# Optimization experiments

Measured on AMD Instinct MI355X. Metric: run time of the kernel, lower is better.

The kernel has to match this reference:

```python
import jax, jax.numpy as jnp
import numpy as np

DIM = 768
HID = 1536
EPS = 1e-12
SCALE = float(np.sqrt(DIM))


def _layernorm(x, gamma, beta):
    mu = jnp.mean(x, axis=-1, keepdims=True)
    var = jnp.mean(jnp.square(x - mu), axis=-1, keepdims=True)
    return (x - mu) * jax.lax.rsqrt(var + EPS) * gamma + beta


def setup_inputs() -> dict:
    key = jax.random.key(0)
    ks = jax.random.split(key, 16)
    s = 1.0 / np.sqrt(DIM)
    sh = 1.0 / np.sqrt(HID)
    x = jax.random.normal(ks[0], (8, 2048, DIM), dtype=jnp.float32)
    return {
        "x": x,
        "Wq": jax.random.uniform(ks[1], (DIM, DIM), jnp.float32, -s, s),
        "bq": jax.random.uniform(ks[2], (DIM,), jnp.float32, -s, s),
        "Wk": jax.random.uniform(ks[3], (DIM, DIM), jnp.float32, -s, s),
        "bk": jax.random.uniform(ks[4], (DIM,), jnp.float32, -s, s),
        "Wv": jax.random.uniform(ks[5], (DIM, DIM), jnp.float32, -s, s),
        "bv": jax.random.uniform(ks[6], (DIM,), jnp.float32, -s, s),
        "Wp": jax.random.uniform(ks[7], (DIM, DIM), jnp.float32, -s, s),
        "bp": jax.random.uniform(ks[8], (DIM,), jnp.float32, -s, s),
        "g1": jnp.ones((DIM,), jnp.float32),
        "be1": jnp.zeros((DIM,), jnp.float32),
        "W1": jax.random.uniform(ks[9], (HID, DIM), jnp.float32, -s, s),
        "b1": jax.random.uniform(ks[10], (HID,), jnp.float32, -s, s),
        "W2": jax.random.uniform(ks[11], (DIM, HID), jnp.float32, -sh, sh),
        "b2": jax.random.uniform(ks[12], (DIM,), jnp.float32, -sh, sh),
        "g2": jnp.ones((DIM,), jnp.float32),
        "be2": jnp.zeros((DIM,), jnp.float32),
    }


def reference(x, Wq, bq, Wk, bk, Wv, bv, Wp, bp, g1, be1, W1, b1, W2, b2, g2, be2):
    # NOTE: original code does NOT split into heads; single full-dim bmm attention.
    Q = jnp.einsum("bsd,ed->bse", x, Wq) + bq  # [B,S,D]
    K = jnp.einsum("bsd,ed->bse", x, Wk) + bk
    V = jnp.einsum("bsd,ed->bse", x, Wv) + bv
    alpha = jnp.einsum("bqd,bkd->bqk", Q, K) / SCALE  # [B,S,S]
    alpha = jax.nn.softmax(alpha, axis=-1)
    attn = jnp.einsum("bqk,bkd->bqd", alpha, V)
    attn = jnp.einsum("bsd,ed->bse", attn, Wp) + bp  # linear_proj
    h = _layernorm(x + attn, g1, be1)
    mlp = jax.nn.gelu(jnp.einsum("bsd,hd->bsh", h, W1) + b1, approximate=False)
    mlp = jnp.einsum("bsh,dh->bsd", mlp, W2) + b2
    return _layernorm(h + mlp, g2, be2)
```

## Files before the change

kernel.cpp:

```cpp
#include <hip/hip_runtime.h>
#include <math.h>

#define D_MODEL 768
#define D_HID   1536
#define N_BATCH 8
#define SEQLEN  2048
#define NROWS   (N_BATCH*SEQLEN)

typedef unsigned short u16;
typedef __attribute__((ext_vector_type(8))) short bfrag;
typedef __attribute__((ext_vector_type(4))) float facc;

__device__ __forceinline__ u16 f2bf(float f) {
  unsigned u = __float_as_uint(f);
  u += 0x7fffu + ((u >> 16) & 1u);
  return (u16)(u >> 16);
}

__device__ __forceinline__ void async16(const void* g, void* l) {
  __builtin_amdgcn_global_load_lds((const __attribute__((address_space(1))) void*)g,
                                   (__attribute__((address_space(3))) void*)l,
                                   16, 0, 0);
}

__global__ __launch_bounds__(256) void cvt_all(
    const float* __restrict__ x,  const float* __restrict__ Wq,
    const float* __restrict__ Wk, const float* __restrict__ Wv,
    const float* __restrict__ Wp, const float* __restrict__ W1,
    const float* __restrict__ W2, const float* __restrict__ bq,
    const float* __restrict__ bk, const float* __restrict__ bv,
    u16* __restrict__ XB, u16* __restrict__ WQKV, u16* __restrict__ WPB,
    u16* __restrict__ W1B, u16* __restrict__ W2B, float* __restrict__ BQKV) {
  long i = (long)blockIdx.x * 256 + threadIdx.x;
  const float* src; u16* dst; long off;
  if      (i < 3145728) { src = x;  dst = XB;             off = i; }
  else if (i < 3293184) { src = Wq; dst = WQKV;           off = i - 3145728; }
  else if (i < 3440640) { src = Wk; dst = WQKV + 589824;  off = i - 3293184; }
  else if (i < 3588096) { src = Wv; dst = WQKV + 1179648; off = i - 3440640; }
  else if (i < 3735552) { src = Wp; dst = WPB;            off = i - 3588096; }
  else if (i < 4030464) { src = W1; dst = W1B;            off = i - 3735552; }
  else if (i < 4325376) { src = W2; dst = W2B;            off = i - 4030464; }
  else if (i < 4325952) {
    long j = i - 4325376;
    const float* s = (j < 192) ? bq : (j < 384) ? bk : bv;
    long o = (j < 192) ? j : (j < 384) ? j - 192 : j - 384;
    ((float4*)BQKV)[j] = ((const float4*)s)[o];
    return;
  } else return;
  float4 v = ((const float4*)src)[off];
  ushort4 o4;
  o4.x = f2bf(v.x); o4.y = f2bf(v.y); o4.z = f2bf(v.z); o4.w = f2bf(v.w);
  *reinterpret_cast<ushort4*>(dst + off * 4) = o4;
}

__global__ __launch_bounds__(256) void transpose_bf16(const u16* __restrict__ in,
                                                      u16* __restrict__ out) {
  __shared__ u16 t[64][68];
  const int z  = blockIdx.z;
  const int bs = blockIdx.x * 64;
  const int bd = blockIdx.y * 64;
  const u16* I = in  + (long)z * SEQLEN * D_MODEL;
  u16*       O = out + (long)z * D_MODEL * SEQLEN;
  const int tt = threadIdx.x;
  const int r = tt >> 2, c4 = (tt & 3) << 4;
#pragma unroll
  for (int k = 0; k < 16; ++k)
    t[r][c4 + k] = I[(long)(bs + r) * D_MODEL + bd + c4 + k];
  __syncthreads();
#pragma unroll
  for (int k = 0; k < 16; ++k)
    O[(long)(bd + r) * SEQLEN + bs + c4 + k] = t[c4 + k][r];
}

enum { EPI_BIAS = 0, EPI_EXP = 1, EPI_DIV = 2, EPI_BIASX = 3, EPI_GELU = 4, EPI_QKV = 5 };

template<int EPI>
__global__ __launch_bounds__(512, 4)
void gemm_bt(const u16* __restrict__ Aall, const u16* __restrict__ Ball,
             void* __restrict__ Cout,
             int M, int N, int K,
             long sA, long sB, long sC,
             const float* __restrict__ bias,
             const float* __restrict__ xadd,
             float* __restrict__ lsum,
             float scale)
{
  __shared__ __align__(16) char smem[65536];
  u16* As = (u16*)smem;
  u16* Bs = (u16*)(smem + 16384);

  const int z = blockIdx.z;
  const u16* A = Aall + (long)z * sA;
  const u16* B = Ball + (long)z * sB;
  const int bm = blockIdx.x, bn = blockIdx.y;
  const int tid = (int)threadIdx.x;
  const int lane = tid & 63, wv = tid >> 6;
  const int wr = wv >> 2, wc = wv & 3;

  facc acc[4][4] = {};

  const int srow = tid >> 3;
  const int scol = (((tid & 7) ^ (srow & 7)) << 3);
  const u16* Abase = A + (long)(bm * 128) * K;
  const u16* Bbase = B + (long)(bn * 256) * K;

  const int fr = lane & 15;
  const int g0 = lane >> 4;

  for (int k0 = 0; k0 < K; k0 += 64) {
    __syncthreads();
#pragma unroll
    for (int p = 0; p < 2; ++p)
      async16(Abase + (long)(p * 64 + srow) * K + k0 + scol, As + (p * 512 + wv * 64) * 8);
#pragma unroll
    for (int p = 0; p < 4; ++p)
      async16(Bbase + (long)(p * 64 + srow) * K + k0 + scol, Bs + (p * 512 + wv * 64) * 8);
    __syncthreads();
#pragma unroll
    for (int h = 0; h < 2; ++h) {
      bfrag af[4], bfv[4];
      const int gh = g0 + h * 4;
      const int cs = (gh ^ (fr & 7)) << 3;
#pragma unroll
      for (int i = 0; i < 4; ++i) {
        const int r = wr * 64 + i * 16 + fr;
        af[i] = *(const bfrag*)(As + r * 64 + ((gh ^ (r & 7)) << 3));
      }
#pragma unroll
      for (int j = 0; j < 4; ++j) {
        const int r = wc * 64 + j * 16 + fr;
        bfv[j] = *(const bfrag*)(Bs + r * 64 + ((gh ^ (r & 7)) << 3));
      }
      (void)cs;
#pragma unroll
      for (int i = 0; i < 4; ++i)
#pragma unroll
        for (int j = 0; j < 4; ++j)
          acc[i][j] = __builtin_amdgcn_mfma_f32_16x16x32_bf16(af[i], bfv[j], acc[i][j], 0, 0, 0);
    }
  }

  __syncthreads();
  const int rb = bm * 128 + wr * 64;
  const int cb = bn * 256 + wc * 64;
  const int quad = lane >> 4;

  if constexpr (EPI == EPI_BIASX) {
    float* ep32 = (float*)(smem + wv * 8192);
    float* Cg = (float*)Cout + (long)z * sC;
#pragma unroll
    for (int h = 0; h < 2; ++h) {
#pragma unroll
      for (int i2 = 0; i2 < 2; ++i2) {
        const int i = h * 2 + i2;
#pragma unroll
        for (int r = 0; r < 4; ++r) {
          const int lrow = i2 * 16 + quad * 4 + r;
#pragma unroll
          for (int j = 0; j < 4; ++j)
            ep32[lrow * 64 + j * 16 + fr] = acc[i][j][r];
        }
      }
#pragma unroll
      for (int it = 0; it < 8; ++it) {
        const int lr = it * 4 + (lane >> 4);
        const int ch = (lane & 15) << 2;
        float4 d = *(const float4*)(ep32 + lr * 64 + ch);
        const int gcol = cb + ch;
        const long gi = (long)(rb + h * 32 + lr) * N + gcol;
        const float4 xa = *(const float4*)(xadd + gi);
        const float4 bb = *(const float4*)(bias + gcol);
        d.x += xa.x + bb.x; d.y += xa.y + bb.y; d.z += xa.z + bb.z; d.w += xa.w + bb.w;
        *(float4*)(Cg + gi) = d;
      }
    }
  } else {
    u16* ep16 = (u16*)(smem + wv * 8192);
    u16* Cg;
    int cbo;
    int rowstride;
    if constexpr (EPI == EPI_QKV) {
      const int c64 = bn * 4 + wc;
      const int which = c64 / 12;
      Cg = (u16*)Cout + (long)which * NROWS * D_MODEL;
      cbo = (c64 - which * 12) * 64;
      rowstride = D_MODEL;
    } else {
      Cg = (u16*)Cout + (long)z * sC;
      cbo = cb;
      rowstride = N;
    }
    float bj[4];
    if constexpr (EPI == EPI_BIAS || EPI == EPI_GELU || EPI == EPI_QKV) {
#pragma unroll
      for (int j = 0; j < 4; ++j) bj[j] = bias[cb + j * 16 + fr];
    }
#pragma unroll
    for (int i = 0; i < 4; ++i) {
#pragma unroll
      for (int r = 0; r < 4; ++r) {
        const int lrow = i * 16 + quad * 4 + r;
        const int row = rb + lrow;
        float rs = 0.f;
        float inv = 0.f;
        if constexpr (EPI == EPI_DIV) inv = 1.f / lsum[(long)z * M + row];
#pragma unroll
        for (int j = 0; j < 4; ++j) {
          float v = acc[i][j][r];
          float outv;
          if constexpr (EPI == EPI_EXP) {
            outv = __expf(v * scale);
            rs += outv;
          } else if constexpr (EPI == EPI_DIV) {
            outv = v * inv;
          } else if constexpr (EPI == EPI_BIAS || EPI == EPI_QKV) {
            outv = v + bj[j];
          } else {
            float t = v + bj[j];
            outv = 0.5f * t * (1.f + erff(t * 0.70710678f));
          }
          ep16[lrow * 64 + j * 16 + fr] = f2bf(outv);
        }
        if constexpr (EPI == EPI_EXP) {
          rs += __shfl_xor(rs, 1);
          rs += __shfl_xor(rs, 2);
          rs += __shfl_xor(rs, 4);
          rs += __shfl_xor(rs, 8);
          if (fr == 0) atomicAdd(&lsum[(long)z * M + row], rs);
        }
      }
    }
#pragma unroll
    for (int it = 0; it < 8; ++it) {
      const int lr = it * 8 + (lane >> 3);
      const int ch = (lane & 7) << 3;
      int4 d = *(const int4*)(ep16 + lr * 64 + ch);
      *reinterpret_cast<int4*>(Cg + (long)(rb + lr) * rowstride + cbo + ch) = d;
    }
  }
}

__global__ __launch_bounds__(256) void layernorm_rows(const float* __restrict__ in,
                                                      const float* __restrict__ gamma,
                                                      const float* __restrict__ beta,
                                                      float* __restrict__ outf,
                                                      u16* __restrict__ outb) {
  const int row = blockIdx.x;
  const float* p = in + (long)row * D_MODEL;
  const int t = threadIdx.x;
  float v0 = p[t], v1 = p[t + 256], v2 = p[t + 512];
  float s1 = v0 + v1 + v2;
  float s2 = v0 * v0 + v1 * v1 + v2 * v2;
#pragma unroll
  for (int o = 32; o; o >>= 1) { s1 += __shfl_xor(s1, o); s2 += __shfl_xor(s2, o); }
  __shared__ float r1[4], r2[4];
  const int wv = t >> 6, ln = t & 63;
  if (ln == 0) { r1[wv] = s1; r2[wv] = s2; }
  __syncthreads();
  s1 = r1[0] + r1[1] + r1[2] + r1[3];
  s2 = r2[0] + r2[1] + r2[2] + r2[3];
  const float mu = s1 * (1.f / 768.f);
  const float var = s2 * (1.f / 768.f) - mu * mu;
  const float rstd = rsqrtf(var + 1e-12f);
  float g0 = gamma[t], g1v = gamma[t + 256], g2v = gamma[t + 512];
  float b0 = beta[t],  b1v = beta[t + 256],  b2v = beta[t + 512];
  float o0 = (v0 - mu) * rstd * g0 + b0;
  float o1 = (v1 - mu) * rstd * g1v + b1v;
  float o2 = (v2 - mu) * rstd * g2v + b2v;
  float* q = outf + (long)row * D_MODEL;
  q[t] = o0; q[t + 256] = o1; q[t + 512] = o2;
  if (outb) {
    u16* qb = outb + (long)row * D_MODEL;
    qb[t] = f2bf(o0); qb[t + 256] = f2bf(o1); qb[t + 512] = f2bf(o2);
  }
}

static const size_t OFF_WP   = 0;
static const size_t OFF_W1   = 1179648;
static const size_t OFF_W2   = 3538944;
static const size_t OFF_LSUM = 5898240;
static const size_t OFF_BQKV = 5963776;
static const size_t OFF_QB   = 6291456;
static const size_t OFF_KB   = 31457280;
static const size_t OFF_VB   = 56623104;
static const size_t OFF_VT   = 81788928;
static const size_t OFF_EB   = 106954752;
static const size_t OFF_XB   = 174063616;
static const size_t OFF_WQKV = 199229440;

extern "C" void kernel_launch(void* const* d_in, const int* in_sizes, int n_in,
                              void* d_out, int out_size, void* d_ws, size_t ws_size,
                              hipStream_t stream) {
  const float* x   = (const float*)d_in[0];
  const float* Wq  = (const float*)d_in[1];
  const float* bq  = (const float*)d_in[2];
  const float* Wk  = (const float*)d_in[3];
  const float* bk  = (const float*)d_in[4];
  const float* Wv  = (const float*)d_in[5];
  const float* bv  = (const float*)d_in[6];
  const float* Wp  = (const float*)d_in[7];
  const float* bp  = (const float*)d_in[8];
  const float* g1  = (const float*)d_in[9];
  const float* be1 = (const float*)d_in[10];
  const float* W1  = (const float*)d_in[11];
  const float* b1  = (const float*)d_in[12];
  const float* W2  = (const float*)d_in[13];
  const float* b2  = (const float*)d_in[14];
  const float* g2  = (const float*)d_in[15];
  const float* be2 = (const float*)d_in[16];

  char* ws = (char*)d_ws;
  u16*   WPB  = (u16*)(ws + OFF_WP);
  u16*   W1B  = (u16*)(ws + OFF_W1);
  u16*   W2B  = (u16*)(ws + OFF_W2);
  float* LSUM = (float*)(ws + OFF_LSUM);
  float* BQKV = (float*)(ws + OFF_BQKV);
  u16*   QB   = (u16*)(ws + OFF_QB);
  u16*   KB   = (u16*)(ws + OFF_KB);
  u16*   VB   = (u16*)(ws + OFF_VB);
  u16*   VT   = (u16*)(ws + OFF_VT);
  u16*   EB   = (u16*)(ws + OFF_EB);
  u16*   XB   = (u16*)(ws + OFF_XB);
  u16*   WQKV = (u16*)(ws + OFF_WQKV);
  u16*   CTX  = (u16*)(ws + OFF_XB);
  float* PF   = (float*)(ws + OFF_QB);
  float* HF   = (float*)(ws + OFF_VB);
  u16*   HB   = (u16*)(ws + OFF_EB);
  u16*   M1B  = (u16*)(ws + OFF_QB);
  float* M2F  = (float*)(ws + OFF_EB);

  dim3 blk(256), blkg(512);

  cvt_all<<<dim3(16899), blk, 0, stream>>>(x, Wq, Wk, Wv, Wp, W1, W2, bq, bk, bv,
                                           XB, WQKV, WPB, W1B, W2B, BQKV);
  hipMemsetAsync(LSUM, 0, NROWS * sizeof(float), stream);

  gemm_bt<EPI_QKV><<<dim3(128, 9, 1), blkg, 0, stream>>>(XB, WQKV, QB,
      NROWS, 3 * D_MODEL, D_MODEL, 0, 0, 0, BQKV, nullptr, nullptr, 0.f);
  transpose_bf16<<<dim3(SEQLEN / 64, D_MODEL / 64, N_BATCH), blk, 0, stream>>>(VB, VT);

  const float sc = 1.0f / sqrtf((float)D_MODEL);
  gemm_bt<EPI_EXP><<<dim3(16, 8, 8), blkg, 0, stream>>>(QB, KB, EB,
      SEQLEN, SEQLEN, D_MODEL,
      (long)SEQLEN * D_MODEL, (long)SEQLEN * D_MODEL, (long)SEQLEN * SEQLEN,
      nullptr, nullptr, LSUM, sc);
  gemm_bt<EPI_DIV><<<dim3(16, 3, 8), blkg, 0, stream>>>(EB, VT, CTX,
      SEQLEN, D_MODEL, SEQLEN,
      (long)SEQLEN * SEQLEN, (long)D_MODEL * SEQLEN, (long)SEQLEN * D_MODEL,
      nullptr, nullptr, LSUM, 0.f);
  gemm_bt<EPI_BIASX><<<dim3(128, 3, 1), blkg, 0, stream>>>(CTX, WPB, PF,
      NROWS, D_MODEL, D_MODEL, 0, 0, 0, bp, x, nullptr, 0.f);
  layernorm_rows<<<dim3(NROWS), blk, 0, stream>>>(PF, g1, be1, HF, HB);
  gemm_bt<EPI_GELU><<<dim3(128, 6, 1), blkg, 0, stream>>>(HB, W1B, M1B,
      NROWS, D_HID, D_MODEL, 0, 0, 0, b1, nullptr, nullptr, 0.f);
  gemm_bt<EPI_BIASX><<<dim3(128, 3, 1), blkg, 0, stream>>>(M1B, W2B, M2F,
      NROWS, D_MODEL, D_HID, 0, 0, 0, b2, HF, nullptr, 0.f);
  layernorm_rows<<<dim3(NROWS), blk, 0, stream>>>(M2F, g2, be2, (float*)d_out, nullptr);

  (void)in_sizes; (void)n_in; (void)out_size; (void)ws_size;
}
```

Before: 518.4 us.

## Use 32x32x16 MFMA, bf16 residual intermediates, and vectorized layernorm

Switches the GEMM inner loop from 16x16x32 to 32x32x16 bf16 MFMA with 2x2 accumulator tiles per wave, cutting LDS fragment loads per MFMA. The projection and MLP-down GEMMs now write bf16 pre-layernorm sums instead of fp32, and they add a bf16 residual (XB or HB) instead of fp32 x/HF. Layernorm reads bf16 with ushort4 vector loads using 192 threads, and the first layernorm no longer writes an fp32 copy. This reduces memory traffic, but it lowers the precision of the residual path and of the layernorm inputs.

```diff
diff --git a/kernel.cpp b/kernel.cpp
--- a/kernel.cpp
+++ b/kernel.cpp
@@ -9,12 +9,15 @@
 
 typedef unsigned short u16;
 typedef __attribute__((ext_vector_type(8))) short bfrag;
-typedef __attribute__((ext_vector_type(4))) float facc;
+typedef __attribute__((ext_vector_type(16))) float facc16;
 
 __device__ __forceinline__ u16 f2bf(float f) {
   unsigned u = __float_as_uint(f);
   u += 0x7fffu + ((u >> 16) & 1u);
   return (u16)(u >> 16);
+}
+__device__ __forceinline__ float bf2f(u16 u) {
+  return __uint_as_float((unsigned)u << 16);
 }
 
 __device__ __forceinline__ void async16(const void* g, void* l) {
@@ -72,7 +75,7 @@
     O[(long)(bd + r) * SEQLEN + bs + c4 + k] = t[c4 + k][r];
 }
 
-enum { EPI_BIAS = 0, EPI_EXP = 1, EPI_DIV = 2, EPI_BIASX = 3, EPI_GELU = 4, EPI_QKV = 5 };
+enum { EPI_EXP = 1, EPI_DIV = 2, EPI_GELU = 4, EPI_QKV = 5, EPI_RES = 6 };
 
 template<int EPI>
 __global__ __launch_bounds__(512, 4)
@@ -81,7 +84,7 @@
              int M, int N, int K,
              long sA, long sB, long sC,
              const float* __restrict__ bias,
-             const float* __restrict__ xadd,
+             const u16* __restrict__ resid,
              float* __restrict__ lsum,
              float scale)
 {
@@ -97,15 +100,15 @@
   const int lane = tid & 63, wv = tid >> 6;
   const int wr = wv >> 2, wc = wv & 3;
 
-  facc acc[4][4] = {};
+  facc16 acc[2][2] = {};
 
   const int srow = tid >> 3;
   const int scol = (((tid & 7) ^ (srow & 7)) << 3);
   const u16* Abase = A + (long)(bm * 128) * K;
   const u16* Bbase = B + (long)(bn * 256) * K;
 
-  const int fr = lane & 15;
-  const int g0 = lane >> 4;
+  const int r32 = lane & 31;
+  const int kh  = lane >> 5;
 
   for (int k0 = 0; k0 < K; k0 += 64) {
     __syncthreads();
@@ -117,68 +120,65 @@
       async16(Bbase + (long)(p * 64 + srow) * K + k0 + scol, Bs + (p * 512 + wv * 64) * 8);
     __syncthreads();
 #pragma unroll
-    for (int h = 0; h < 2; ++h) {
-      bfrag af[4], bfv[4];
-      const int gh = g0 + h * 4;
-      const int cs = (gh ^ (fr & 7)) << 3;
-#pragma unroll
-      for (int i = 0; i < 4; ++i) {
-        const int r = wr * 64 + i * 16 + fr;
-        af[i] = *(const bfrag*)(As + r * 64 + ((gh ^ (r & 7)) << 3));
-      }
-#pragma unroll
-      for (int j = 0; j < 4; ++j) {
-        const int r = wc * 64 + j * 16 + fr;
-        bfv[j] = *(const bfrag*)(Bs + r * 64 + ((gh ^ (r & 7)) << 3));
-      }
-      (void)cs;
-#pragma unroll
-      for (int i = 0; i < 4; ++i)
-#pragma unroll
-        for (int j = 0; j < 4; ++j)
-          acc[i][j] = __builtin_amdgcn_mfma_f32_16x16x32_bf16(af[i], bfv[j], acc[i][j], 0, 0, 0);
+    for (int s = 0; s < 4; ++s) {
+      bfrag af[2], bfv[2];
+      const int kc = s * 2 + kh;
+#pragma unroll
+      for (int i2 = 0; i2 < 2; ++i2) {
+        const int r = wr * 64 + i2 * 32 + r32;
+        af[i2] = *(const bfrag*)(As + r * 64 + ((kc ^ (r & 7)) << 3));
+      }
+#pragma unroll
+      for (int j2 = 0; j2 < 2; ++j2) {
+        const int r = wc * 64 + j2 * 32 + r32;
+        bfv[j2] = *(const bfrag*)(Bs + r * 64 + ((kc ^ (r & 7)) << 3));
+      }
+#pragma unroll
+      for (int i2 = 0; i2 < 2; ++i2)
+#pragma unroll
+        for (int j2 = 0; j2 < 2; ++j2)
+          acc[i2][j2] = __builtin_amdgcn_mfma_f32_32x32x16_bf16(af[i2], bfv[j2], acc[i2][j2], 0, 0, 0);
     }
   }
 
   __syncthreads();
   const int rb = bm * 128 + wr * 64;
   const int cb = bn * 256 + wc * 64;
-  const int quad = lane >> 4;
-
-  if constexpr (EPI == EPI_BIASX) {
+
+  if constexpr (EPI == EPI_RES) {
     float* ep32 = (float*)(smem + wv * 8192);
-    float* Cg = (float*)Cout + (long)z * sC;
+    u16* Cg = (u16*)Cout;
 #pragma unroll
     for (int h = 0; h < 2; ++h) {
 #pragma unroll
-      for (int i2 = 0; i2 < 2; ++i2) {
-        const int i = h * 2 + i2;
-#pragma unroll
-        for (int r = 0; r < 4; ++r) {
-          const int lrow = i2 * 16 + quad * 4 + r;
-#pragma unroll
-          for (int j = 0; j < 4; ++j)
-            ep32[lrow * 64 + j * 16 + fr] = acc[i][j][r];
-        }
+      for (int reg = 0; reg < 16; ++reg) {
+        const int lrow = (reg & 3) + 8 * (reg >> 2) + 4 * kh;
+#pragma unroll
+        for (int j2 = 0; j2 < 2; ++j2)
+          ep32[lrow * 64 + j2 * 32 + r32] = acc[h][j2][reg];
       }
 #pragma unroll
       for (int it = 0; it < 8; ++it) {
         const int lr = it * 4 + (lane >> 4);
         const int ch = (lane & 15) << 2;
         float4 d = *(const float4*)(ep32 + lr * 64 + ch);
+        const int row = rb + h * 32 + lr;
         const int gcol = cb + ch;
-        const long gi = (long)(rb + h * 32 + lr) * N + gcol;
-        const float4 xa = *(const float4*)(xadd + gi);
-        const float4 bb = *(const float4*)(bias + gcol);
-        d.x += xa.x + bb.x; d.y += xa.y + bb.y; d.z += xa.z + bb.z; d.w += xa.w + bb.w;
-        *(float4*)(Cg + gi) = d;
+        const long gi = (long)row * N + gcol;
+        ushort4 rv = *(const ushort4*)(resid + gi);
+        float4 bb = *(const float4*)(bias + gcol);
+        ushort4 o;
+        o.x = f2bf(d.x + bb.x + bf2f(rv.x));
+        o.y = f2bf(d.y + bb.y + bf2f(rv.y));
+        o.z = f2bf(d.z + bb.z + bf2f(rv.z));
+        o.w = f2bf(d.w + bb.w + bf2f(rv.w));
+        *reinterpret_cast<ushort4*>(Cg + gi) = o;
       }
     }
   } else {
     u16* ep16 = (u16*)(smem + wv * 8192);
     u16* Cg;
-    int cbo;
-    int rowstride;
+    int cbo, rowstride;
     if constexpr (EPI == EPI_QKV) {
       const int c64 = bn * 4 + wc;
       const int which = c64 / 12;
@@ -190,43 +190,44 @@
       cbo = cb;
       rowstride = N;
     }
-    float bj[4];
-    if constexpr (EPI == EPI_BIAS || EPI == EPI_GELU || EPI == EPI_QKV) {
-#pragma unroll
-      for (int j = 0; j < 4; ++j) bj[j] = bias[cb + j * 16 + fr];
-    }
-#pragma unroll
-    for (int i = 0; i < 4; ++i) {
-#pragma unroll
-      for (int r = 0; r < 4; ++r) {
-        const int lrow = i * 16 + quad * 4 + r;
+    float bj[2];
+    if constexpr (EPI == EPI_GELU || EPI == EPI_QKV) {
+#pragma unroll
+      for (int j2 = 0; j2 < 2; ++j2) bj[j2] = bias[cb + j2 * 32 + r32];
+    }
+#pragma unroll
+    for (int i2 = 0; i2 < 2; ++i2) {
+#pragma unroll
+      for (int reg = 0; reg < 16; ++reg) {
+        const int lrow = i2 * 32 + (reg & 3) + 8 * (reg >> 2) + 4 * kh;
         const int row = rb + lrow;
         float rs = 0.f;
         float inv = 0.f;
         if constexpr (EPI == EPI_DIV) inv = 1.f / lsum[(long)z * M + row];
 #pragma unroll
-        for (int j = 0; j < 4; ++j) {
-          float v = acc[i][j][r];
+        for (int j2 = 0; j2 < 2; ++j2) {
+          float v = acc[i2][j2][reg];
           float outv;
           if constexpr (EPI == EPI_EXP) {
             outv = __expf(v * scale);
             rs += outv;
           } else if constexpr (EPI == EPI_DIV) {
             outv = v * inv;
-          } else if constexpr (EPI == EPI_BIAS || EPI == EPI_QKV) {
-            outv = v + bj[j];
+          } else if constexpr (EPI == EPI_QKV) {
+            outv = v + bj[j2];
           } else {
-            float t = v + bj[j];
+            float t = v + bj[j2];
             outv = 0.5f * t * (1.f + erff(t * 0.70710678f));
           }
-          ep16[lrow * 64 + j * 16 + fr] = f2bf(outv);
+          ep16[lrow * 64 + j2 * 32 + r32] = f2bf(outv);
         }
         if constexpr (EPI == EPI_EXP) {
           rs += __shfl_xor(rs, 1);
           rs += __shfl_xor(rs, 2);
           rs += __shfl_xor(rs, 4);
           rs += __shfl_xor(rs, 8);
-          if (fr == 0) atomicAdd(&lsum[(long)z * M + row], rs);
+          rs += __shfl_xor(rs, 16);
+          if (r32 == 0) atomicAdd(&lsum[(long)z * M + row], rs);
         }
       }
     }
@@ -240,38 +241,42 @@
   }
 }
 
-__global__ __launch_bounds__(256) void layernorm_rows(const float* __restrict__ in,
+__global__ __launch_bounds__(192) void layernorm_rows(const u16* __restrict__ in,
                                                       const float* __restrict__ gamma,
                                                       const float* __restrict__ beta,
                                                       float* __restrict__ outf,
                                                       u16* __restrict__ outb) {
   const int row = blockIdx.x;
-  const float* p = in + (long)row * D_MODEL;
   const int t = threadIdx.x;
-  float v0 = p[t], v1 = p[t + 256], v2 = p[t + 512];
-  float s1 = v0 + v1 + v2;
-  float s2 = v0 * v0 + v1 * v1 + v2 * v2;
+  ushort4 uv = ((const ushort4*)(in + (long)row * D_MODEL))[t];
+  float v0 = bf2f(uv.x), v1 = bf2f(uv.y), v2 = bf2f(uv.z), v3 = bf2f(uv.w);
+  float s1 = v0 + v1 + v2 + v3;
+  float s2 = v0 * v0 + v1 * v1 + v2 * v2 + v3 * v3;
 #pragma unroll
   for (int o = 32; o; o >>= 1) { s1 += __shfl_xor(s1, o); s2 += __shfl_xor(s2, o); }
-  __shared__ float r1[4], r2[4];
+  __shared__ float r1[3], r2[3];
   const int wv = t >> 6, ln = t & 63;
   if (ln == 0) { r1[wv] = s1; r2[wv] = s2; }
   __syncthreads();
-  s1 = r1[0] + r1[1] + r1[2] + r1[3];
-  s2 = r2[0] + r2[1] + r2[2] + r2[3];
+  s1 = r1[0] + r1[1] + r1[2];
+  s2 = r2[0] + r2[1] + r2[2];
   const float mu = s1 * (1.f / 768.f);
   const float var = s2 * (1.f / 768.f) - mu * mu;
   const float rstd = rsqrtf(var + 1e-12f);
-  float g0 = gamma[t], g1v = gamma[t + 256], g2v = gamma[t + 512];
-  float b0 = beta[t],  b1v = beta[t + 256],  b2v = beta[t + 512];
-  float o0 = (v0 - mu) * rstd * g0 + b0;
-  float o1 = (v1 - mu) * rstd * g1v + b1v;
-  float o2 = (v2 - mu) * rstd * g2v + b2v;
-  float* q = outf + (long)row * D_MODEL;
-  q[t] = o0; q[t + 256] = o1; q[t + 512] = o2;
+  float4 gv = ((const float4*)gamma)[t];
+  float4 bv = ((const float4*)beta)[t];
+  float o0 = (v0 - mu) * rstd * gv.x + bv.x;
+  float o1 = (v1 - mu) * rstd * gv.y + bv.y;
+  float o2 = (v2 - mu) * rstd * gv.z + bv.z;
+  float o3 = (v3 - mu) * rstd * gv.w + bv.w;
+  if (outf) {
+    float4 ov = {o0, o1, o2, o3};
+    ((float4*)(outf + (long)row * D_MODEL))[t] = ov;
+  }
   if (outb) {
-    u16* qb = outb + (long)row * D_MODEL;
-    qb[t] = f2bf(o0); qb[t + 256] = f2bf(o1); qb[t + 512] = f2bf(o2);
+    ushort4 ob;
+    ob.x = f2bf(o0); ob.y = f2bf(o1); ob.z = f2bf(o2); ob.w = f2bf(o3);
+    ((ushort4*)(outb + (long)row * D_MODEL))[t] = ob;
   }
 }
 
@@ -322,14 +327,13 @@
   u16*   EB   = (u16*)(ws + OFF_EB);
   u16*   XB   = (u16*)(ws + OFF_XB);
   u16*   WQKV = (u16*)(ws + OFF_WQKV);
-  u16*   CTX  = (u16*)(ws + OFF_XB);
-  float* PF   = (float*)(ws + OFF_QB);
-  float* HF   = (float*)(ws + OFF_VB);
+  u16*   CTX  = (u16*)(ws + OFF_VB);
+  u16*   PB   = (u16*)(ws + OFF_QB);
   u16*   HB   = (u16*)(ws + OFF_EB);
   u16*   M1B  = (u16*)(ws + OFF_QB);
-  float* M2F  = (float*)(ws + OFF_EB);
-
-  dim3 blk(256), blkg(512);
+  u16*   M2B  = (u16*)(ws + OFF_VT);
+
+  dim3 blk(256), blkg(512), blkl(192);
 
   cvt_all<<<dim3(16899), blk, 0, stream>>>(x, Wq, Wk, Wv, Wp, W1, W2, bq, bk, bv,
                                            XB, WQKV, WPB, W1B, W2B, BQKV);
@@ -348,14 +352,14 @@
       SEQLEN, D_MODEL, SEQLEN,
       (long)SEQLEN * SEQLEN, (long)D_MODEL * SEQLEN, (long)SEQLEN * D_MODEL,
       nullptr, nullptr, LSUM, 0.f);
-  gemm_bt<EPI_BIASX><<<dim3(128, 3, 1), blkg, 0, stream>>>(CTX, WPB, PF,
-      NROWS, D_MODEL, D_MODEL, 0, 0, 0, bp, x, nullptr, 0.f);
-  layernorm_rows<<<dim3(NROWS), blk, 0, stream>>>(PF, g1, be1, HF, HB);
+  gemm_bt<EPI_RES><<<dim3(128, 3, 1), blkg, 0, stream>>>(CTX, WPB, PB,
+      NROWS, D_MODEL, D_MODEL, 0, 0, 0, bp, XB, nullptr, 0.f);
+  layernorm_rows<<<dim3(NROWS), blkl, 0, stream>>>(PB, g1, be1, nullptr, HB);
   gemm_bt<EPI_GELU><<<dim3(128, 6, 1), blkg, 0, stream>>>(HB, W1B, M1B,
       NROWS, D_HID, D_MODEL, 0, 0, 0, b1, nullptr, nullptr, 0.f);
-  gemm_bt<EPI_BIASX><<<dim3(128, 3, 1), blkg, 0, stream>>>(M1B, W2B, M2F,
-      NROWS, D_MODEL, D_HID, 0, 0, 0, b2, HF, nullptr, 0.f);
-  layernorm_rows<<<dim3(NROWS), blk, 0, stream>>>(M2F, g2, be2, (float*)d_out, nullptr);
+  gemm_bt<EPI_RES><<<dim3(128, 3, 1), blkg, 0, stream>>>(M1B, W2B, M2B,
+      NROWS, D_MODEL, D_HID, 0, 0, 0, b2, HB, nullptr, 0.f);
+  layernorm_rows<<<dim3(NROWS), blkl, 0, stream>>>(M2B, g2, be2, (float*)d_out, nullptr);
 
   (void)in_sizes; (void)n_in; (void)out_size; (void)ws_size;
 }
```

Measured after the change: 528.2 us. No clear change (+1.9%).
